# Performance work log

Measured on AMD Instinct MI355X. Metric: run time of the kernel, lower is better.

The kernel has to match this reference:

```python
import jax, jax.numpy as jnp
import numpy as np

NL = 4      # nl
H = 256     # h_size
F = 128     # input_size (Fourier features); mapping output = 2*F
DIM = 3     # self.dim
N = 4096    # rows of coords; effective batch after vstack = 2*N


def setup_inputs() -> dict:
    key = jax.random.key(0)
    ks = jax.random.split(key, 7)
    coords = jax.random.normal(ks[0], (N, 2 * DIM), jnp.float32)
    B = jax.random.normal(ks[1], (DIM, F), jnp.float32)            # Fourier mapping matrix
    w0 = jax.random.normal(ks[2], (H, 2 * F), jnp.float32) * 0.1   # encoder[0].weight
    ws = jax.random.normal(ks[3], (NL - 1, H, H), jnp.float32) * 0.1   # encoder[1..nl-1].weight
    w_last = jax.random.normal(ks[4], (H, H), jnp.float32) * 0.1   # encoder[-1].weight
    w1 = jax.random.normal(ks[5], (NL, H, H), jnp.float32) * 0.1   # encoder1[ii].weight
    b1 = jax.random.normal(ks[6], (NL, H), jnp.float32) * 0.1      # encoder1[ii].bias
    return dict(coords=coords, B=B, w0=w0, ws=ws, w_last=w_last, w1=w1, b1=b1)


def input_mapping(x, B):
    # FBPINNs Fourier feature mapping: [sin(2*pi*x@B), cos(2*pi*x@B)]
    proj = (2.0 * jnp.pi) * (x @ B)                  # (2N, F)
    return jnp.concatenate([jnp.sin(proj), jnp.cos(proj)], axis=-1)  # (2N, 2F)


def sin_layer(x, w):
    # y[b,j] = sum_k sin(x[b,k] * w[j,k])  -- broadcast multiply + sin + reduce
    return jnp.sin(x[:, None, :] * w[None, :, :]).sum(axis=2)


def reference(coords, B, w0, ws, w_last, w1, b1):
    x0 = coords[:, :DIM]
    x1 = coords[:, DIM:]
    x = jnp.concatenate([x0, x1], axis=0)            # vstack -> (2N, DIM)
    x = input_mapping(x, B)                          # (2N, 2F)
    x = sin_layer(x, w0)                             # (2N, H)
    x = jnp.sin(x @ w1[0].T + b1[0])                 # encoder1[0] + sin
    for ii in range(1, NL):
        x = sin_layer(x, ws[ii - 1])                 # encoder[ii] sin-layer
        x = jnp.sin(x @ w1[ii].T + b1[ii])           # encoder1[ii] + sin
    x = sin_layer(x, w_last)                         # encoder[-1] sin-layer
    return (x, coords)
```

## Files before the change

### kernel.cpp

```cpp
#include <hip/hip_runtime.h>
#include <string.h>

#define NCRD 4096
#define NROW 8192
#define MT   32
#define WG_U4 114688

typedef __attribute__((ext_vector_type(8))) _Float16 half8;
typedef __attribute__((ext_vector_type(4))) float f32x4;

static __device__ __forceinline__ float sinrev(float t){ return __builtin_amdgcn_sinf(__builtin_amdgcn_fractf(t)); }
static __device__ __forceinline__ float cosrev(float t){ return __builtin_amdgcn_cosf(__builtin_amdgcn_fractf(t)); }
static __device__ __forceinline__ unsigned short f2h(float f){
    _Float16 h = (_Float16)f;
    unsigned short u; memcpy(&u, &h, 2); return u;
}

__constant__ int c_offs[9] = {0,16384,24576,40960,49152,65536,73728,90112,98304};

__global__ void prep_kernel(const float* __restrict__ w0, const float* __restrict__ ws,
                            const float* __restrict__ wlast, const float* __restrict__ w1,
                            const float* __restrict__ coords, const float* __restrict__ b1,
                            uint4* __restrict__ Wg, float* __restrict__ b1s,
                            float* __restrict__ out)
{
    int l = blockIdx.x, part = blockIdx.y, t = threadIdx.x;
    const float inv2pi = 0.15915494309189535f;
    if (l == 9) {
        int base = part*256 + t;
        if (base < 1024) b1s[base] = b1[base]*inv2pi;
        for (int i = base; i < NCRD*6; i += 16384)
            out[(size_t)NROW*256 + i] = coords[i];
        return;
    }
    bool sinl = !(l & 1);
    if (!sinl && part >= 32) return;
    const float* src;
    switch (l) {
        case 0: src = w0;          break;
        case 1: src = w1;          break;
        case 2: src = ws;          break;
        case 3: src = w1+65536;    break;
        case 4: src = ws+65536;    break;
        case 5: src = w1+2*65536;  break;
        case 6: src = ws+2*65536;  break;
        case 7: src = w1+3*65536;  break;
        default: src = wlast;      break;
    }
    int idx = part*256 + t;
    int c  = idx >> 10, r = idx & 1023;
    int q  = r >> 7,  r2 = r & 127;
    int tt = r2 >> 6;
    int lq = (r2 >> 4) & 3, lr = r2 & 15;
    int col  = q*32 + tt*16 + lr;
    int keff = c*32 + lq*8;
    int term = keff >> 8, kk = keff & 255;
    const float* s = src + col*256 + kk;
    unsigned short h[8];
    #pragma unroll
    for (int j = 0; j < 8; ++j) {
        float w = s[j], v;
        if (!sinl)          v = w * inv2pi;
        else if (term == 0) v = w;
        else                v = -w*w*w*(1.0f/6.0f);
        h[j] = f2h(v);
    }
    uint4 o; memcpy(&o, h, 16);
    Wg[c_offs[l] + idx] = o;
}

template<int MODE, int NC>
static __device__ __forceinline__ void do_layer(
    const uint4* __restrict__ wq,
    const float* __restrict__ br,
    float* __restrict__ outg,
    unsigned short* xa,
    int wv, int lq, int lr, int n0)
{
    constexpr int PD = 8;
    constexpr int PA = 2;
    f32x4 acc00 = {0.f,0.f,0.f,0.f}, acc01 = acc00, acc10 = acc00, acc11 = acc00;

    uint4 pu0[PD], pu1[PD];
    #pragma unroll
    for (int p = 0; p < PD; ++p) {
        if (p < NC) { pu0[p] = wq[p*1024]; pu1[p] = wq[p*1024 + 64]; }
    }
    float bb0 = 0.f, bb1 = 0.f;
    if (MODE == 1) { bb0 = br[wv*32 + lr]; bb1 = br[wv*32 + 16 + lr]; }

    __syncthreads();
    const half8* xa8 = (const half8*)xa;
    half8 pa0[PA], pa1[PA];
    #pragma unroll
    for (int p = 0; p < PA; ++p) {
        pa0[p] = xa8[(p*4 + lq)*32 + lr];
        pa1[p] = xa8[(p*4 + lq)*32 + 16 + lr];
    }
    #pragma unroll
    for (int c = 0; c < NC; ++c) {
        half8 b0, b1v;
        { uint4 t0 = pu0[c % PD], t1 = pu1[c % PD];
          memcpy(&b0, &t0, 16); memcpy(&b1v, &t1, 16); }
        half8 a0 = pa0[c % PA], a1 = pa1[c % PA];
        if (c + PD < NC) {
            pu0[c % PD] = wq[(c+PD)*1024];
            pu1[c % PD] = wq[(c+PD)*1024 + 64];
        }
        if (c + PA < NC) {
            pa0[c % PA] = xa8[((c+PA)*4 + lq)*32 + lr];
            pa1[c % PA] = xa8[((c+PA)*4 + lq)*32 + 16 + lr];
        }
        acc00 = __builtin_amdgcn_mfma_f32_16x16x32_f16(a0, b0,  acc00, 0,0,0);
        acc01 = __builtin_amdgcn_mfma_f32_16x16x32_f16(a0, b1v, acc01, 0,0,0);
        acc10 = __builtin_amdgcn_mfma_f32_16x16x32_f16(a1, b0,  acc10, 0,0,0);
        acc11 = __builtin_amdgcn_mfma_f32_16x16x32_f16(a1, b1v, acc11, 0,0,0);
    }
    __syncthreads();
    #pragma unroll
    for (int rt = 0; rt < 2; ++rt)
        #pragma unroll
        for (int ct = 0; ct < 2; ++ct) {
            f32x4 A = rt==0 ? (ct==0?acc00:acc01) : (ct==0?acc10:acc11);
            int h = wv*32 + ct*16 + lr;
            float bb = ct==0 ? bb0 : bb1;
            #pragma unroll
            for (int r = 0; r < 4; ++r) {
                float v = A[r];
                int m = rt*16 + lq*4 + r;
                if (MODE == 2) {
                    outg[(size_t)(n0 + m)*256 + h] = v;
                } else if (MODE == 1) {
                    float s = sinrev(v + bb);
                    float s3 = s*s*s;
                    xa[(((h>>3)     )*32 + m)*8 + (h&7)] = f2h(s);
                    xa[(((h>>3) + 32)*32 + m)*8 + (h&7)] = f2h(s3);
                } else {
                    xa[((h>>3)*32 + m)*8 + (h&7)] = f2h(v);
                }
            }
        }
}

__global__ __launch_bounds__(512, 2)
void net_kernel(const float* __restrict__ coords, const float* __restrict__ Bm,
                const uint4* __restrict__ Wg, const float* __restrict__ b1s,
                float* __restrict__ out)
{
    __shared__ unsigned short xa[64*32*8];
    __shared__ float cb[MT*3];
    __shared__ float bl[384];

    int tid = threadIdx.x, lane = tid & 63, wv = tid >> 6;
    int lq = lane >> 4, lr = lane & 15;
    int n0 = blockIdx.x * MT;

    for (int i = tid; i < MT*3; i += 512) {
        int r = i/3, d = i - 3*r, nv = n0 + r;
        cb[i] = (nv < NCRD) ? coords[nv*6 + d] : coords[(nv-NCRD)*6 + 3 + d];
    }
    for (int i = tid; i < 384; i += 512) bl[i] = Bm[i];
    __syncthreads();
    {
        int m = tid & 31, colb = (tid >> 5) * 16;
        float c0 = cb[m*3], c1 = cb[m*3+1], c2 = cb[m*3+2];
        unsigned short tmp[2][16];
        #pragma unroll
        for (int j = 0; j < 16; ++j) {
            int col = colb + j, f = col & 127;
            float p = c0*bl[f] + c1*bl[128+f] + c2*bl[256+f];
            float s = (col < 128) ? sinrev(p) : cosrev(p);
            tmp[0][j] = f2h(s); tmp[1][j] = f2h(s*s*s);
        }
        #pragma unroll
        for (int pp = 0; pp < 2; ++pp)
            #pragma unroll
            for (int g = 0; g < 2; ++g) {
                uint4 v; memcpy(&v, &tmp[pp][g*8], 16);
                *(uint4*)&xa[((pp*32 + (colb>>3) + g)*32 + m)*8] = v;
            }
    }

    int wl = wv*128 + lane;
    do_layer<0,16>(Wg +      0 + wl, nullptr,   nullptr, xa, wv, lq, lr, n0);
    do_layer<1, 8>(Wg +  16384 + wl, b1s + 0,   nullptr, xa, wv, lq, lr, n0);
    do_layer<0,16>(Wg +  24576 + wl, nullptr,   nullptr, xa, wv, lq, lr, n0);
    do_layer<1, 8>(Wg +  40960 + wl, b1s + 256, nullptr, xa, wv, lq, lr, n0);
    do_layer<0,16>(Wg +  49152 + wl, nullptr,   nullptr, xa, wv, lq, lr, n0);
    do_layer<1, 8>(Wg +  65536 + wl, b1s + 512, nullptr, xa, wv, lq, lr, n0);
    do_layer<0,16>(Wg +  73728 + wl, nullptr,   nullptr, xa, wv, lq, lr, n0);
    do_layer<1, 8>(Wg +  90112 + wl, b1s + 768, nullptr, xa, wv, lq, lr, n0);
    do_layer<2,16>(Wg +  98304 + wl, nullptr,   out,     xa, wv, lq, lr, n0);
}

extern "C" void kernel_launch(void* const* d_in, const int* in_sizes, int n_in,
                              void* d_out, int out_size, void* d_ws, size_t ws_size,
                              hipStream_t stream)
{
    const float* coords = (const float*)d_in[0];
    const float* Bm     = (const float*)d_in[1];
    const float* w0     = (const float*)d_in[2];
    const float* ws     = (const float*)d_in[3];
    const float* wlast  = (const float*)d_in[4];
    const float* w1     = (const float*)d_in[5];
    const float* b1     = (const float*)d_in[6];
    float* out = (float*)d_out;

    uint4* Wg  = (uint4*)d_ws;
    float* b1s = (float*)((char*)d_ws + (size_t)WG_U4*16);

    dim3 pg(10, 64);
    prep_kernel<<<pg, 256, 0, stream>>>(w0, ws, wlast, w1, coords, b1, Wg, b1s, out);
    net_kernel<<<NROW/MT, 512, 0, stream>>>(coords, Bm, Wg, b1s, out);
}
```

Baseline: 102.7 us.

## Double workgroup to 16 waves with one column tile each and asm-managed weight prefetch ring

Each workgroup now runs 1024 threads (16 waves), and each wave computes a single 16-column tile instead of two, halving per-wave accumulators and weight loads. Weight prefetch moves to inline-asm global_load_dwordx4 into a 9-slot ring, with explicit s_waitcnt vmcnt counts so loads are waited on one at a time instead of relying on compiler scheduling. The Fourier feature prologue is re-split so each thread handles 8 columns. The aim is more latency hiding through more waves and finer-grained memory waits, at the cost of more barrier participants, possible register pressure under launch_bounds(1024,4), and fragile hand-written waitcnt that assumes no other outstanding vector-memory ops.

```diff
diff --git a/kernel.cpp b/kernel.cpp
--- a/kernel.cpp
+++ b/kernel.cpp
@@ -8,12 +8,30 @@
 
 typedef __attribute__((ext_vector_type(8))) _Float16 half8;
 typedef __attribute__((ext_vector_type(4))) float f32x4;
+typedef __attribute__((ext_vector_type(4))) int   i32x4;
 
 static __device__ __forceinline__ float sinrev(float t){ return __builtin_amdgcn_sinf(__builtin_amdgcn_fractf(t)); }
 static __device__ __forceinline__ float cosrev(float t){ return __builtin_amdgcn_cosf(__builtin_amdgcn_fractf(t)); }
 static __device__ __forceinline__ unsigned short f2h(float f){
     _Float16 h = (_Float16)f;
     unsigned short u; memcpy(&u, &h, 2); return u;
+}
+
+static __device__ __forceinline__ i32x4 gload16(const uint4* p){
+    i32x4 r;
+    asm volatile("global_load_dwordx4 %0, %1, off" : "=v"(r) : "v"(p) : "memory");
+    return r;
+}
+static __device__ __forceinline__ void vmwaitK(int K, i32x4& a){
+    if (K >= 8)      asm volatile("s_waitcnt vmcnt(8)" : "+v"(a));
+    else if (K == 7) asm volatile("s_waitcnt vmcnt(7)" : "+v"(a));
+    else if (K == 6) asm volatile("s_waitcnt vmcnt(6)" : "+v"(a));
+    else if (K == 5) asm volatile("s_waitcnt vmcnt(5)" : "+v"(a));
+    else if (K == 4) asm volatile("s_waitcnt vmcnt(4)" : "+v"(a));
+    else if (K == 3) asm volatile("s_waitcnt vmcnt(3)" : "+v"(a));
+    else if (K == 2) asm volatile("s_waitcnt vmcnt(2)" : "+v"(a));
+    else if (K == 1) asm volatile("s_waitcnt vmcnt(1)" : "+v"(a));
+    else             asm volatile("s_waitcnt vmcnt(0)" : "+v"(a));
 }
 
 __constant__ int c_offs[9] = {0,16384,24576,40960,49152,65536,73728,90112,98304};
@@ -78,16 +96,14 @@
     int wv, int lq, int lr, int n0)
 {
     constexpr int PD = 8;
+    constexpr int RS = PD + 1;
     constexpr int PA = 2;
-    f32x4 acc00 = {0.f,0.f,0.f,0.f}, acc01 = acc00, acc10 = acc00, acc11 = acc00;
-
-    uint4 pu0[PD], pu1[PD];
-    #pragma unroll
-    for (int p = 0; p < PD; ++p) {
-        if (p < NC) { pu0[p] = wq[p*1024]; pu1[p] = wq[p*1024 + 64]; }
-    }
-    float bb0 = 0.f, bb1 = 0.f;
-    if (MODE == 1) { bb0 = br[wv*32 + lr]; bb1 = br[wv*32 + 16 + lr]; }
+    f32x4 acc0 = {0.f,0.f,0.f,0.f}, acc1 = acc0;
+
+    i32x4 ring[RS];
+    #pragma unroll
+    for (int p = 0; p < PD; ++p)
+        if (p < NC) ring[p % RS] = gload16(wq + p*1024);
 
     __syncthreads();
     const half8* xa8 = (const half8*)xa;
@@ -99,50 +115,45 @@
     }
     #pragma unroll
     for (int c = 0; c < NC; ++c) {
-        half8 b0, b1v;
-        { uint4 t0 = pu0[c % PD], t1 = pu1[c % PD];
-          memcpy(&b0, &t0, 16); memcpy(&b1v, &t1, 16); }
-        half8 a0 = pa0[c % PA], a1 = pa1[c % PA];
-        if (c + PD < NC) {
-            pu0[c % PD] = wq[(c+PD)*1024];
-            pu1[c % PD] = wq[(c+PD)*1024 + 64];
-        }
+        if (c + PD < NC)
+            ring[(c+PD) % RS] = gload16(wq + (c+PD)*1024);
+        int K = NC-1-c;
+        vmwaitK(K > PD ? PD : K, ring[c % RS]);
+        half8 b0, a0 = pa0[c % PA], a1 = pa1[c % PA];
+        { i32x4 t0 = ring[c % RS]; memcpy(&b0, &t0, 16); }
         if (c + PA < NC) {
             pa0[c % PA] = xa8[((c+PA)*4 + lq)*32 + lr];
             pa1[c % PA] = xa8[((c+PA)*4 + lq)*32 + 16 + lr];
         }
-        acc00 = __builtin_amdgcn_mfma_f32_16x16x32_f16(a0, b0,  acc00, 0,0,0);
-        acc01 = __builtin_amdgcn_mfma_f32_16x16x32_f16(a0, b1v, acc01, 0,0,0);
-        acc10 = __builtin_amdgcn_mfma_f32_16x16x32_f16(a1, b0,  acc10, 0,0,0);
-        acc11 = __builtin_amdgcn_mfma_f32_16x16x32_f16(a1, b1v, acc11, 0,0,0);
+        acc0 = __builtin_amdgcn_mfma_f32_16x16x32_f16(a0, b0, acc0, 0,0,0);
+        acc1 = __builtin_amdgcn_mfma_f32_16x16x32_f16(a1, b0, acc1, 0,0,0);
     }
     __syncthreads();
-    #pragma unroll
-    for (int rt = 0; rt < 2; ++rt)
+    float bb = 0.f;
+    if (MODE == 1) bb = br[wv*16 + lr];
+    int h = wv*16 + lr;
+    #pragma unroll
+    for (int rt = 0; rt < 2; ++rt) {
+        f32x4 A = rt==0 ? acc0 : acc1;
         #pragma unroll
-        for (int ct = 0; ct < 2; ++ct) {
-            f32x4 A = rt==0 ? (ct==0?acc00:acc01) : (ct==0?acc10:acc11);
-            int h = wv*32 + ct*16 + lr;
-            float bb = ct==0 ? bb0 : bb1;
-            #pragma unroll
-            for (int r = 0; r < 4; ++r) {
-                float v = A[r];
-                int m = rt*16 + lq*4 + r;
-                if (MODE == 2) {
-                    outg[(size_t)(n0 + m)*256 + h] = v;
-                } else if (MODE == 1) {
-                    float s = sinrev(v + bb);
-                    float s3 = s*s*s;
-                    xa[(((h>>3)     )*32 + m)*8 + (h&7)] = f2h(s);
-                    xa[(((h>>3) + 32)*32 + m)*8 + (h&7)] = f2h(s3);
-                } else {
-                    xa[((h>>3)*32 + m)*8 + (h&7)] = f2h(v);
-                }
+        for (int r = 0; r < 4; ++r) {
+            float v = A[r];
+            int m = rt*16 + lq*4 + r;
+            if (MODE == 2) {
+                outg[(size_t)(n0 + m)*256 + h] = v;
+            } else if (MODE == 1) {
+                float s = sinrev(v + bb);
+                float s3 = s*s*s;
+                xa[(((h>>3)     )*32 + m)*8 + (h&7)] = f2h(s);
+                xa[(((h>>3) + 32)*32 + m)*8 + (h&7)] = f2h(s3);
+            } else {
+                xa[((h>>3)*32 + m)*8 + (h&7)] = f2h(v);
             }
         }
-}
-
-__global__ __launch_bounds__(512, 2)
+    }
+}
+
+__global__ __launch_bounds__(1024, 4)
 void net_kernel(const float* __restrict__ coords, const float* __restrict__ Bm,
                 const uint4* __restrict__ Wg, const float* __restrict__ b1s,
                 float* __restrict__ out)
@@ -155,33 +166,31 @@
     int lq = lane >> 4, lr = lane & 15;
     int n0 = blockIdx.x * MT;
 
-    for (int i = tid; i < MT*3; i += 512) {
-        int r = i/3, d = i - 3*r, nv = n0 + r;
-        cb[i] = (nv < NCRD) ? coords[nv*6 + d] : coords[(nv-NCRD)*6 + 3 + d];
-    }
-    for (int i = tid; i < 384; i += 512) bl[i] = Bm[i];
+    if (tid < MT*3) {
+        int r = tid/3, d = tid - 3*r, nv = n0 + r;
+        cb[tid] = (nv < NCRD) ? coords[nv*6 + d] : coords[(nv-NCRD)*6 + 3 + d];
+    }
+    if (tid < 384) bl[tid] = Bm[tid];
     __syncthreads();
     {
-        int m = tid & 31, colb = (tid >> 5) * 16;
+        int m = tid & 31, cg = tid >> 5;
         float c0 = cb[m*3], c1 = cb[m*3+1], c2 = cb[m*3+2];
-        unsigned short tmp[2][16];
+        unsigned short tmp[2][8];
         #pragma unroll
-        for (int j = 0; j < 16; ++j) {
-            int col = colb + j, f = col & 127;
+        for (int j = 0; j < 8; ++j) {
+            int col = cg*8 + j, f = col & 127;
             float p = c0*bl[f] + c1*bl[128+f] + c2*bl[256+f];
             float s = (col < 128) ? sinrev(p) : cosrev(p);
             tmp[0][j] = f2h(s); tmp[1][j] = f2h(s*s*s);
         }
         #pragma unroll
-        for (int pp = 0; pp < 2; ++pp)
-            #pragma unroll
-            for (int g = 0; g < 2; ++g) {
-                uint4 v; memcpy(&v, &tmp[pp][g*8], 16);
-                *(uint4*)&xa[((pp*32 + (colb>>3) + g)*32 + m)*8] = v;
-            }
-    }
-
-    int wl = wv*128 + lane;
+        for (int pp = 0; pp < 2; ++pp) {
+            uint4 v; memcpy(&v, &tmp[pp][0], 16);
+            *(uint4*)&xa[((pp*32 + cg)*32 + m)*8] = v;
+        }
+    }
+
+    int wl = wv*64 + lane;
     do_layer<0,16>(Wg +      0 + wl, nullptr,   nullptr, xa, wv, lq, lr, n0);
     do_layer<1, 8>(Wg +  16384 + wl, b1s + 0,   nullptr, xa, wv, lq, lr, n0);
     do_layer<0,16>(Wg +  24576 + wl, nullptr,   nullptr, xa, wv, lq, lr, n0);
@@ -211,5 +220,5 @@
 
     dim3 pg(10, 64);
     prep_kernel<<<pg, 256, 0, stream>>>(w0, ws, wlast, w1, coords, b1, Wg, b1s, out);
-    net_kernel<<<NROW/MT, 512, 0, stream>>>(coords, Bm, Wg, b1s, out);
-}
+    net_kernel<<<NROW/MT, 1024, 0, stream>>>(coords, Bm, Wg, b1s, out);
+}
```

After: 96.63 us. 1.06x faster.
